# Performance work log

Hardware: AMD Instinct MI355X
Metric: run time of the kernel (lower is better)

The kernel has to match this reference:

```python
import jax, jax.numpy as jnp
import numpy as np

T, B, E = 1024, 4, 1024
H = 16
D = E // H          # head_dim = 64
L = 16              # max_relative_length


def setup_inputs() -> dict:
    key = jax.random.key(0)
    ks = jax.random.split(key, 4)
    query = jax.random.normal(ks[0], (T, B, E), dtype=jnp.float32)
    # xavier-ish scaled params
    in_proj_weight = jax.random.normal(ks[1], (3 * E, E), dtype=jnp.float32) * (1.0 / np.sqrt(E))
    in_proj_bias = jnp.zeros((3 * E,), dtype=jnp.float32)
    rel_pos_keys = jax.random.normal(ks[2], (2 * L + 1, E), dtype=jnp.float32) * (1.0 / np.sqrt(E))
    out_w = jax.random.normal(ks[3], (E, E), dtype=jnp.float32) * (1.0 / np.sqrt(E))
    out_b = jnp.zeros((E,), dtype=jnp.float32)
    return {"query": query, "in_proj_weight": in_proj_weight, "in_proj_bias": in_proj_bias,
            "rel_pos_keys": rel_pos_keys, "out_w": out_w, "out_b": out_b}


def reference(query, in_proj_weight, in_proj_bias, rel_pos_keys, out_w, out_b):
    t, b, e = query.shape
    scaling = D ** (-0.5)
    # fused qkv projection: [T,B,3E]
    qkv = jnp.einsum('tbe,fe->tbf', query, in_proj_weight) + in_proj_bias
    q, k, v = jnp.split(qkv, 3, axis=-1)
    q = q * scaling
    # [T,B,E] -> [B*H, T, D]
    def heads(x):
        return x.reshape(t, b * H, D).transpose(1, 0, 2)
    q, k, v = heads(q), heads(k), heads(v)
    # clipped relative position matrix [T,T] in [0, 2L]
    r = jnp.arange(t)
    dist = jnp.clip(r[None, :] - r[:, None], -L, L) + L
    # gather relation keys, keep first head_dim channels: [T,T,D]
    rel_k = rel_pos_keys[dist][:, :, :D]
    # scores = q k^T + q . rel_k  (Shaw et al.), [B*H, T, T]
    scores = jnp.einsum('btd,bsd->bts', q, k) + jnp.einsum('btd,tsd->bts', q, rel_k)
    probs = jax.nn.softmax(scores, axis=-1)
    attn = jnp.einsum('bts,bsd->btd', probs, v)      # [B*H, T, D]
    attn = attn.transpose(1, 0, 2).reshape(t, b, e)   # [T, B, E]
    return jnp.einsum('tbe,oe->tbo', attn, out_w) + out_b
```

## Files before the change

kernel.cpp:

```cpp
#include <hip/hip_runtime.h>

typedef __attribute__((ext_vector_type(8))) short short8;
typedef __attribute__((ext_vector_type(4))) float floatx4;


__device__ __forceinline__ short f2bf(float x) {
  union { float f; unsigned u; } cv; cv.f = x;
  unsigned u = cv.u + (0x7FFFu + ((cv.u >> 16) & 1u));
  return (short)(u >> 16);
}

__device__ __forceinline__ floatx4 mfma16(short8 a, short8 b, floatx4 c) {
  return __builtin_amdgcn_mfma_f32_16x16x32_bf16(a, b, c, 0, 0, 0);
}

__device__ __forceinline__ void async_copy16(const void* g, void* l) {
  __builtin_amdgcn_global_load_lds((const __attribute__((address_space(1))) void*)g,
                                   (__attribute__((address_space(3))) void*)l, 16, 0, 0);
}

__global__ void __launch_bounds__(256) convert_all_kernel(
    const float* __restrict__ s0, const float* __restrict__ s1,
    const float* __restrict__ s2,
    short* __restrict__ d0, short* __restrict__ d1, short* __restrict__ d2)
{
  int i = blockIdx.x * 256 + threadIdx.x;
  const float* src; short* dst; int off;
  if (i < 524288)       { src = s0; dst = d0; off = i; }
  else if (i < 917504)  { src = s1; dst = d1; off = i - 524288; }
  else                  { src = s2; dst = d2; off = i - 917504; }
  const float4* s = (const float4*)src;
  float4 a = s[off * 2], b = s[off * 2 + 1];
  short8 o;
  o[0] = f2bf(a.x); o[1] = f2bf(a.y); o[2] = f2bf(a.z); o[3] = f2bf(a.w);
  o[4] = f2bf(b.x); o[5] = f2bf(b.y); o[6] = f2bf(b.z); o[7] = f2bf(b.w);
  *(short8*)(dst + (size_t)off * 8) = o;
}

__device__ __forceinline__ void gemm_stage(
    const short* __restrict__ A, const short* __restrict__ W,
    short* Atile, short* Btile, int m0, int n0, int K, int kk, int tid, int w)
{
  #pragma unroll
  for (int i = 0; i < 2; i++) {
    int seg = i * 256 + tid;
    int row = seg >> 2, c = seg & 3;
    async_copy16(A + (size_t)(m0 + row) * K + kk + c * 8,
                 Atile + (size_t)(i * 256 + w * 64) * 8);
    async_copy16(W + (size_t)(n0 + row) * K + kk + c * 8,
                 Btile + (size_t)(i * 256 + w * 64) * 8);
  }
}

__device__ __forceinline__ void gemm_core_db(
    const short* __restrict__ A, const short* __restrict__ W,
    short* At, short* Bt,
    int m0, int n0, int K, int tid, floatx4 acc[4][4])
{
  const int lane = tid & 63, w = tid >> 6;
  const int quad = lane >> 4, l16 = lane & 15;
  const int wm = (w >> 1) * 64, wn = (w & 1) * 64;
  #pragma unroll
  for (int mt = 0; mt < 4; mt++)
    #pragma unroll
    for (int nt = 0; nt < 4; nt++) acc[mt][nt] = (floatx4)(0.0f);

  gemm_stage(A, W, At, Bt, m0, n0, K, 0, tid, w);

  for (int kk = 0; kk < K; kk += 32) {
    const int cur = (kk >> 5) & 1;
    short* Ac = At + cur * (128 * 32);
    short* Bc = Bt + cur * (128 * 32);
    __syncthreads();
    if (kk + 32 < K)
      gemm_stage(A, W, At + (1 - cur) * (128 * 32), Bt + (1 - cur) * (128 * 32),
                 m0, n0, K, kk + 32, tid, w);
    short8 af[4], bfr[4];
    #pragma unroll
    for (int mt = 0; mt < 4; mt++)
      af[mt] = *(const short8*)(Ac + (wm + mt * 16 + l16) * 32 + quad * 8);
    #pragma unroll
    for (int nt = 0; nt < 4; nt++)
      bfr[nt] = *(const short8*)(Bc + (wn + nt * 16 + l16) * 32 + quad * 8);
    #pragma unroll
    for (int mt = 0; mt < 4; mt++)
      #pragma unroll
      for (int nt = 0; nt < 4; nt++)
        acc[mt][nt] = mfma16(af[mt], bfr[nt], acc[mt][nt]);
  }
}

__global__ void __launch_bounds__(256) gemm_qkv(
    const short* __restrict__ A, const short* __restrict__ W,
    const float* __restrict__ bias,
    short* __restrict__ q_ws, short* __restrict__ k_ws, short* __restrict__ v_ws)
{
  __shared__ __align__(16) short Atile[2 * 128 * 32];
  __shared__ __align__(16) short Btile[2 * 128 * 32];
  const int tid = threadIdx.x;
  const int m0 = blockIdx.x * 128, n0 = blockIdx.y * 128;
  floatx4 acc[4][4];
  gemm_core_db(A, W, Atile, Btile, m0, n0, 1024, tid, acc);

  const int lane = tid & 63, w = tid >> 6;
  const int quad = lane >> 4, l16 = lane & 15;
  const int wm = (w >> 1) * 64, wn = (w & 1) * 64;
  #pragma unroll
  for (int nt = 0; nt < 4; nt++) {
    int f = n0 + wn + nt * 16 + l16;
    float bv = bias[f];
    int which = f >> 10;
    int h = (f >> 6) & 15;
    int d = f & 63;
    #pragma unroll
    for (int mt = 0; mt < 4; mt++) {
      #pragma unroll
      for (int reg = 0; reg < 4; reg++) {
        int r = m0 + wm + mt * 16 + quad * 4 + reg;
        int t = r >> 2, b = r & 3;
        int bh = b * 16 + h;
        float val = acc[mt][nt][reg] + bv;
        if (which == 0)      q_ws[((size_t)bh * 1024 + t) * 64 + d] = f2bf(val * 0.125f);
        else if (which == 1) k_ws[((size_t)bh * 1024 + t) * 64 + d] = f2bf(val);
        else                 v_ws[((size_t)bh * 64 + d) * 1024 + t] = f2bf(val);
      }
    }
  }
}

__global__ void __launch_bounds__(256) attn_kernel(
    const short* __restrict__ q_ws, const short* __restrict__ k_ws,
    const short* __restrict__ v_ws, const float* __restrict__ relk,
    short* __restrict__ attn_ws)
{
  __shared__ float rel_lds[64 * 33];
  __shared__ __align__(16) short Ktile[2][64 * 64];
  __shared__ __align__(16) short Vtile[2][64 * 64];
  __shared__ __align__(16) short p_lds[4][16 * 64];
  const int tid = threadIdx.x, lane = tid & 63, w = tid >> 6;
  const int quad = lane >> 4, l16 = lane & 15;
  const int bh = blockIdx.x >> 4;
  const int t0 = (blockIdx.x & 15) * 64;
  const int b = bh >> 4, h = bh & 15;

  short8 aq[2];
  #pragma unroll
  for (int ks = 0; ks < 2; ks++)
    aq[ks] = *(const short8*)(q_ws + ((size_t)bh * 1024 + t0 + w * 16 + l16) * 64
                              + ks * 32 + quad * 8);

  for (int i = tid; i < 48 * 8; i += 256) {
    int row = i >> 3, p = i & 7;
    short8 val;
    if (row < 33) {
      const float* src = relk + row * 1024 + p * 8;
      float4 a = *(const float4*)src, c = *(const float4*)(src + 4);
      val[0] = f2bf(a.x); val[1] = f2bf(a.y); val[2] = f2bf(a.z); val[3] = f2bf(a.w);
      val[4] = f2bf(c.x); val[5] = f2bf(c.y); val[6] = f2bf(c.z); val[7] = f2bf(c.w);
    } else {
      val = (short8)0;
    }
    *(short8*)(Ktile[0] + row * 64 + ((p ^ (row & 7)) << 3)) = val;
  }
  __syncthreads();

  #pragma unroll
  for (int jt = 0; jt < 3; jt++) {
    floatx4 scR = (floatx4)(0.0f);
    #pragma unroll
    for (int ks = 0; ks < 2; ks++) {
      int rrow = jt * 16 + l16;
      int ck = (quad + 4 * ks) ^ (rrow & 7);
      short8 rb = *(const short8*)(Ktile[0] + rrow * 64 + ck * 8);
      scR = mfma16(aq[ks], rb, scR);
    }
    int j = jt * 16 + l16;
    if (j < 33) {
      #pragma unroll
      for (int reg = 0; reg < 4; reg++) {
        int tl = w * 16 + quad * 4 + reg;
        rel_lds[tl * 33 + j] = scR[reg];
      }
    }
  }
  __syncthreads();

  const int qloc = w * 16 + l16;
  const float biasLo = rel_lds[qloc * 33 + 0];
  const float biasHi = rel_lds[qloc * 33 + 32];

  floatx4 o[4];
  #pragma unroll
  for (int dt = 0; dt < 4; dt++) o[dt] = (floatx4)(0.0f);
  float rsum = 0.f;

  const short* kg = k_ws + (size_t)bh * 1024 * 64;
  const short* vg = v_ws + (size_t)bh * 64 * 1024;

  #define STAGE_KV(S0, BUF)                                                  \
    {                                                                        \
      _Pragma("unroll")                                                      \
      for (int i = 0; i < 2; i++) {                                          \
        int seg = i * 256 + tid;                                             \
        int row = seg >> 3, p = seg & 7;                                     \
        int ck = p ^ (row & 7);                                              \
        async_copy16(kg + (size_t)((S0) + row) * 64 + ck * 8,                \
                     Ktile[BUF] + (size_t)(i * 256 + w * 64) * 8);           \
        async_copy16(vg + (size_t)row * 1024 + (S0) + ck * 8,                \
                     Vtile[BUF] + (size_t)(i * 256 + w * 64) * 8);           \
      }                                                                      \
    }

  STAGE_KV(0, 0);

  for (int st = 0; st < 16; st++) {
    const int s0 = st * 64;
    const int cur = st & 1;
    __syncthreads();
    if (st < 15) STAGE_KV(s0 + 64, 1 - cur);

    floatx4 sc[4];
    #pragma unroll
    for (int nt = 0; nt < 4; nt++) {
      sc[nt] = (floatx4)(0.0f);
      #pragma unroll
      for (int ks = 0; ks < 2; ks++) {
        int srow = nt * 16 + l16;
        int ck = (quad + 4 * ks) ^ (l16 & 7);
        short8 kb = *(const short8*)(Ktile[cur] + srow * 64 + ck * 8);
        sc[nt] = mfma16(kb, aq[ks], sc[nt]);
      }
    }

    bool alllo = (s0 <= t0 + w * 16 - 79);
    bool allhi = (s0 >= t0 + w * 16 + 31);
    if (alllo || allhi) {
      float bb = alllo ? biasLo : biasHi;
      #pragma unroll
      for (int nt = 0; nt < 4; nt++)
        #pragma unroll
        for (int reg = 0; reg < 4; reg++) sc[nt][reg] += bb;
    } else {
      #pragma unroll
      for (int nt = 0; nt < 4; nt++) {
        #pragma unroll
        for (int reg = 0; reg < 4; reg++) {
          int delta = (s0 + 16 * nt + 4 * quad + reg) - (t0 + qloc);
          delta = min(max(delta, -16), 16) + 16;
          sc[nt][reg] += rel_lds[qloc * 33 + delta];
        }
      }
    }

    #pragma unroll
    for (int nt = 0; nt < 4; nt++) {
      #pragma unroll
      for (int reg = 0; reg < 4; reg++) {
        float p = __expf(sc[nt][reg]);
        sc[nt][reg] = p;
        rsum += p;
      }
      unsigned w0 = (unsigned)(unsigned short)f2bf(sc[nt][0])
                  | ((unsigned)(unsigned short)f2bf(sc[nt][1]) << 16);
      unsigned w1 = (unsigned)(unsigned short)f2bf(sc[nt][2])
                  | ((unsigned)(unsigned short)f2bf(sc[nt][3]) << 16);
      int srot = (16 * nt + 4 * quad + 4 * l16) & 63;
      *(uint2*)(p_lds[w] + l16 * 64 + srot) = make_uint2(w0, w1);
    }

    short8 ap[2];
    #pragma unroll
    for (int ks = 0; ks < 2; ks++) {
      int s1 = (32 * ks + 8 * quad + 4 * l16) & 63;
      int s2 = (s1 + 4) & 63;
      union { short8 v; uint2 u[2]; } pu;
      pu.u[0] = *(const uint2*)(p_lds[w] + l16 * 64 + s1);
      pu.u[1] = *(const uint2*)(p_lds[w] + l16 * 64 + s2);
      ap[ks] = pu.v;
    }

    #pragma unroll
    for (int dt = 0; dt < 4; dt++) {
      #pragma unroll
      for (int ks = 0; ks < 2; ks++) {
        int drow = dt * 16 + l16;
        int ck = (quad + 4 * ks) ^ (l16 & 7);
        short8 vb = *(const short8*)(Vtile[cur] + drow * 64 + ck * 8);
        o[dt] = mfma16(ap[ks], vb, o[dt]);
      }
    }
  }
  #undef STAGE_KV

  rsum += __shfl_xor(rsum, 16, 64);
  rsum += __shfl_xor(rsum, 32, 64);
  float inv[4];
  #pragma unroll
  for (int reg = 0; reg < 4; reg++)
    inv[reg] = 1.0f / __shfl(rsum, quad * 4 + reg, 64);
  #pragma unroll
  for (int dt = 0; dt < 4; dt++) {
    #pragma unroll
    for (int reg = 0; reg < 4; reg++) {
      int tg = t0 + w * 16 + quad * 4 + reg;
      attn_ws[((size_t)tg * 4 + b) * 1024 + h * 64 + dt * 16 + l16]
        = f2bf(o[dt][reg] * inv[reg]);
    }
  }
}

__global__ void __launch_bounds__(256) gemm_outproj(
    const short* __restrict__ A, const short* __restrict__ W,
    const float* __restrict__ bias, float* __restrict__ out)
{
  __shared__ __align__(16) short Atile[2 * 64 * 32];
  __shared__ __align__(16) short Btile[2 * 128 * 32];
  const int tid = threadIdx.x;
  const int m0 = blockIdx.x * 64, n0 = blockIdx.y * 128;
  const int lane = tid & 63, w = tid >> 6;
  const int quad = lane >> 4, l16 = lane & 15;
  const int wm = (w >> 1) * 32, wn = (w & 1) * 64;

  floatx4 acc[2][4];
  #pragma unroll
  for (int mt = 0; mt < 2; mt++)
    #pragma unroll
    for (int nt = 0; nt < 4; nt++) acc[mt][nt] = (floatx4)(0.0f);

  #define STAGE_OP(KK, BUF)                                                  \
    {                                                                        \
      _Pragma("unroll")                                                      \
      for (int i = 0; i < 2; i++) {                                          \
        int seg = i * 256 + tid;                \
        int row = seg >> 2, c = seg & 3;                                     \
        async_copy16(W + (size_t)(n0 + row) * 1024 + (KK) + c * 8,           \
                     Btile + (size_t)((BUF) * 4096 + (i * 256 + w * 64) * 8)); \
      }                                                                      \
      {                                                                      \
        int row = tid >> 2, c = tid & 3;         \
        async_copy16(A + (size_t)(m0 + row) * 1024 + (KK) + c * 8,           \
                     Atile + (size_t)((BUF) * 2048 + (w * 64) * 8));         \
      }                                                                      \
    }

  STAGE_OP(0, 0);
  for (int kk = 0; kk < 1024; kk += 32) {
    const int cur = (kk >> 5) & 1;
    const short* Ac = Atile + cur * 2048;
    const short* Bc = Btile + cur * 4096;
    __syncthreads();
    if (kk + 32 < 1024) STAGE_OP(kk + 32, 1 - cur);
    short8 af[2], bfr[4];
    #pragma unroll
    for (int mt = 0; mt < 2; mt++)
      af[mt] = *(const short8*)(Ac + (wm + mt * 16 + l16) * 32 + quad * 8);
    #pragma unroll
    for (int nt = 0; nt < 4; nt++)
      bfr[nt] = *(const short8*)(Bc + (wn + nt * 16 + l16) * 32 + quad * 8);
    #pragma unroll
    for (int mt = 0; mt < 2; mt++)
      #pragma unroll
      for (int nt = 0; nt < 4; nt++)
        acc[mt][nt] = mfma16(af[mt], bfr[nt], acc[mt][nt]);
  }
  #undef STAGE_OP

  #pragma unroll
  for (int nt = 0; nt < 4; nt++) {
    int f = n0 + wn + nt * 16 + l16;
    float bv = bias[f];
    #pragma unroll
    for (int mt = 0; mt < 2; mt++) {
      #pragma unroll
      for (int reg = 0; reg < 4; reg++) {
        int r = m0 + wm + mt * 16 + quad * 4 + reg;
        out[(size_t)r * 1024 + f] = acc[mt][nt][reg] + bv;
      }
    }
  }
}

extern "C" void kernel_launch(void* const* d_in, const int* in_sizes, int n_in,
                              void* d_out, int out_size, void* d_ws, size_t ws_size,
                              hipStream_t stream) {
  const float* query = (const float*)d_in[0];
  const float* in_w  = (const float*)d_in[1];
  const float* in_b  = (const float*)d_in[2];
  const float* relk  = (const float*)d_in[3];
  const float* out_w = (const float*)d_in[4];
  const float* out_b = (const float*)d_in[5];
  float* out = (float*)d_out;

  short* qry_bf = (short*)d_ws;
  short* win_bf = qry_bf + (size_t)4096 * 1024;
  short* wout_bf = win_bf + (size_t)3072 * 1024;
  short* q_ws   = wout_bf + (size_t)1024 * 1024;
  short* k_ws   = q_ws + (size_t)64 * 1024 * 64;
  short* v_ws   = k_ws + (size_t)64 * 1024 * 64;
  short* att_ws = v_ws + (size_t)64 * 1024 * 64;

  convert_all_kernel<<<4096, 256, 0, stream>>>(query, in_w, out_w,
                                               qry_bf, win_bf, wout_bf);
  gemm_qkv<<<dim3(32, 24), 256, 0, stream>>>(qry_bf, win_bf, in_b, q_ws, k_ws, v_ws);
  attn_kernel<<<1024, 256, 0, stream>>>(q_ws, k_ws, v_ws, relk, att_ws);
  gemm_outproj<<<dim3(64, 8), 256, 0, stream>>>(att_ws, wout_bf, out_b, out);
}
```

Baseline: 188.6 us.

## Double query rows per attention block and swizzle GEMM LDS tiles

The attention kernel now handles 128 query rows per block (two 16-row tiles per wave), so each K/V tile loaded into LDS feeds twice as many MFMAs, and the grid drops to 512 blocks. K/V double buffering is removed in favour of a single buffer with a sync at the end of each iteration, which serialises the loads with compute. Separately, both GEMMs apply a rotation swizzle to LDS tile columns to reduce bank conflicts on fragment reads. The trade-offs are higher register pressure, fewer blocks, and lost load/compute overlap in attention.

```diff
diff --git a/kernel.cpp b/kernel.cpp
--- a/kernel.cpp
+++ b/kernel.cpp
@@ -44,10 +44,11 @@
   #pragma unroll
   for (int i = 0; i < 2; i++) {
     int seg = i * 256 + tid;
-    int row = seg >> 2, c = seg & 3;
-    async_copy16(A + (size_t)(m0 + row) * K + kk + c * 8,
+    int row = seg >> 2, p = seg & 3;
+    int ck = (p - ((row >> 1) & 3)) & 3;
+    async_copy16(A + (size_t)(m0 + row) * K + kk + ck * 8,
                  Atile + (size_t)(i * 256 + w * 64) * 8);
-    async_copy16(W + (size_t)(n0 + row) * K + kk + c * 8,
+    async_copy16(W + (size_t)(n0 + row) * K + kk + ck * 8,
                  Btile + (size_t)(i * 256 + w * 64) * 8);
   }
 }
@@ -77,11 +78,15 @@
                  m0, n0, K, kk + 32, tid, w);
     short8 af[4], bfr[4];
     #pragma unroll
-    for (int mt = 0; mt < 4; mt++)
-      af[mt] = *(const short8*)(Ac + (wm + mt * 16 + l16) * 32 + quad * 8);
-    #pragma unroll
-    for (int nt = 0; nt < 4; nt++)
-      bfr[nt] = *(const short8*)(Bc + (wn + nt * 16 + l16) * 32 + quad * 8);
+    for (int mt = 0; mt < 4; mt++) {
+      int R = wm + mt * 16 + l16;
+      af[mt] = *(const short8*)(Ac + R * 32 + ((quad + (R >> 1)) & 3) * 8);
+    }
+    #pragma unroll
+    for (int nt = 0; nt < 4; nt++) {
+      int R = wn + nt * 16 + l16;
+      bfr[nt] = *(const short8*)(Bc + R * 32 + ((quad + (R >> 1)) & 3) * 8);
+    }
     #pragma unroll
     for (int mt = 0; mt < 4; mt++)
       #pragma unroll
@@ -133,21 +138,24 @@
     const short* __restrict__ v_ws, const float* __restrict__ relk,
     short* __restrict__ attn_ws)
 {
-  __shared__ float rel_lds[64 * 33];
-  __shared__ __align__(16) short Ktile[2][64 * 64];
-  __shared__ __align__(16) short Vtile[2][64 * 64];
-  __shared__ __align__(16) short p_lds[4][16 * 64];
+  __shared__ float rel_lds[128 * 33];
+  __shared__ __align__(16) short Ktile[64 * 64];
+  __shared__ __align__(16) short Vtile[64 * 64];
+  __shared__ __align__(16) short p_lds[4][32 * 64];
   const int tid = threadIdx.x, lane = tid & 63, w = tid >> 6;
   const int quad = lane >> 4, l16 = lane & 15;
-  const int bh = blockIdx.x >> 4;
-  const int t0 = (blockIdx.x & 15) * 64;
+  const int bh = blockIdx.x >> 3;
+  const int t0 = (blockIdx.x & 7) * 128;
   const int b = bh >> 4, h = bh & 15;
 
-  short8 aq[2];
-  #pragma unroll
-  for (int ks = 0; ks < 2; ks++)
-    aq[ks] = *(const short8*)(q_ws + ((size_t)bh * 1024 + t0 + w * 16 + l16) * 64
-                              + ks * 32 + quad * 8);
+  short8 aq[2][2];
+  #pragma unroll
+  for (int qt = 0; qt < 2; qt++)
+    #pragma unroll
+    for (int ks = 0; ks < 2; ks++)
+      aq[qt][ks] = *(const short8*)(q_ws
+          + ((size_t)bh * 1024 + t0 + qt * 64 + w * 16 + l16) * 64
+          + ks * 32 + quad * 8);
 
   for (int i = tid; i < 48 * 8; i += 256) {
     int row = i >> 3, p = i & 7;
@@ -160,151 +168,174 @@
     } else {
       val = (short8)0;
     }
-    *(short8*)(Ktile[0] + row * 64 + ((p ^ (row & 7)) << 3)) = val;
+    *(short8*)(Ktile + row * 64 + ((p ^ (row & 7)) << 3)) = val;
   }
   __syncthreads();
 
   #pragma unroll
-  for (int jt = 0; jt < 3; jt++) {
-    floatx4 scR = (floatx4)(0.0f);
-    #pragma unroll
-    for (int ks = 0; ks < 2; ks++) {
-      int rrow = jt * 16 + l16;
-      int ck = (quad + 4 * ks) ^ (rrow & 7);
-      short8 rb = *(const short8*)(Ktile[0] + rrow * 64 + ck * 8);
-      scR = mfma16(aq[ks], rb, scR);
-    }
-    int j = jt * 16 + l16;
-    if (j < 33) {
-      #pragma unroll
-      for (int reg = 0; reg < 4; reg++) {
-        int tl = w * 16 + quad * 4 + reg;
-        rel_lds[tl * 33 + j] = scR[reg];
+  for (int qt = 0; qt < 2; qt++) {
+    #pragma unroll
+    for (int jt = 0; jt < 3; jt++) {
+      floatx4 scR = (floatx4)(0.0f);
+      #pragma unroll
+      for (int ks = 0; ks < 2; ks++) {
+        int rrow = jt * 16 + l16;
+        int ck = (quad + 4 * ks) ^ (rrow & 7);
+        short8 rb = *(const short8*)(Ktile + rrow * 64 + ck * 8);
+        scR = mfma16(aq[qt][ks], rb, scR);
+      }
+      int j = jt * 16 + l16;
+      if (j < 33) {
+        #pragma unroll
+        for (int reg = 0; reg < 4; reg++) {
+          int tl = qt * 64 + w * 16 + quad * 4 + reg;
+          rel_lds[tl * 33 + j] = scR[reg];
+        }
       }
     }
   }
   __syncthreads();
 
-  const int qloc = w * 16 + l16;
-  const float biasLo = rel_lds[qloc * 33 + 0];
-  const float biasHi = rel_lds[qloc * 33 + 32];
-
-  floatx4 o[4];
-  #pragma unroll
-  for (int dt = 0; dt < 4; dt++) o[dt] = (floatx4)(0.0f);
-  float rsum = 0.f;
+  float biasLo[2], biasHi[2];
+  #pragma unroll
+  for (int qt = 0; qt < 2; qt++) {
+    int ql = qt * 64 + w * 16 + l16;
+    biasLo[qt] = rel_lds[ql * 33 + 0];
+    biasHi[qt] = rel_lds[ql * 33 + 32];
+  }
+
+  floatx4 o[2][4];
+  #pragma unroll
+  for (int qt = 0; qt < 2; qt++)
+    #pragma unroll
+    for (int dt = 0; dt < 4; dt++) o[qt][dt] = (floatx4)(0.0f);
+  float rsum[2] = {0.f, 0.f};
 
   const short* kg = k_ws + (size_t)bh * 1024 * 64;
   const short* vg = v_ws + (size_t)bh * 64 * 1024;
 
-  #define STAGE_KV(S0, BUF)                                                  \
-    {                                                                        \
-      _Pragma("unroll")                                                      \
-      for (int i = 0; i < 2; i++) {                                          \
-        int seg = i * 256 + tid;                                             \
-        int row = seg >> 3, p = seg & 7;                                     \
-        int ck = p ^ (row & 7);                                              \
-        async_copy16(kg + (size_t)((S0) + row) * 64 + ck * 8,                \
-                     Ktile[BUF] + (size_t)(i * 256 + w * 64) * 8);           \
-        async_copy16(vg + (size_t)row * 1024 + (S0) + ck * 8,                \
-                     Vtile[BUF] + (size_t)(i * 256 + w * 64) * 8);           \
-      }                                                                      \
-    }
-
-  STAGE_KV(0, 0);
-
   for (int st = 0; st < 16; st++) {
     const int s0 = st * 64;
-    const int cur = st & 1;
+    #pragma unroll
+    for (int i = 0; i < 2; i++) {
+      int seg = i * 256 + tid;
+      int row = seg >> 3, p = seg & 7;
+      int ck = p ^ (row & 7);
+      async_copy16(kg + (size_t)(s0 + row) * 64 + ck * 8,
+                   Ktile + (size_t)(i * 256 + w * 64) * 8);
+      async_copy16(vg + (size_t)row * 1024 + s0 + ck * 8,
+                   Vtile + (size_t)(i * 256 + w * 64) * 8);
+    }
     __syncthreads();
-    if (st < 15) STAGE_KV(s0 + 64, 1 - cur);
-
-    floatx4 sc[4];
-    #pragma unroll
-    for (int nt = 0; nt < 4; nt++) {
-      sc[nt] = (floatx4)(0.0f);
+
+    short8 kb[4][2];
+    #pragma unroll
+    for (int nt = 0; nt < 4; nt++)
       #pragma unroll
       for (int ks = 0; ks < 2; ks++) {
         int srow = nt * 16 + l16;
-        int ck = (quad + 4 * ks) ^ (l16 & 7);
-        short8 kb = *(const short8*)(Ktile[cur] + srow * 64 + ck * 8);
-        sc[nt] = mfma16(kb, aq[ks], sc[nt]);
-      }
-    }
-
-    bool alllo = (s0 <= t0 + w * 16 - 79);
-    bool allhi = (s0 >= t0 + w * 16 + 31);
-    if (alllo || allhi) {
-      float bb = alllo ? biasLo : biasHi;
-      #pragma unroll
-      for (int nt = 0; nt < 4; nt++)
-        #pragma unroll
-        for (int reg = 0; reg < 4; reg++) sc[nt][reg] += bb;
-    } else {
+        kb[nt][ks] = *(const short8*)(Ktile + srow * 64
+                                      + (((quad + 4 * ks) ^ (l16 & 7)) << 3));
+      }
+
+    floatx4 sc[2][4];
+    #pragma unroll
+    for (int qt = 0; qt < 2; qt++)
       #pragma unroll
       for (int nt = 0; nt < 4; nt++) {
+        sc[qt][nt] = (floatx4)(0.0f);
+        #pragma unroll
+        for (int ks = 0; ks < 2; ks++)
+          sc[qt][nt] = mfma16(kb[nt][ks], aq[qt][ks], sc[qt][nt]);
+      }
+
+    #pragma unroll
+    for (int qt = 0; qt < 2; qt++) {
+      const int qbase = t0 + qt * 64 + w * 16;
+      bool alllo = (s0 <= qbase - 79);
+      bool allhi = (s0 >= qbase + 31);
+      if (alllo || allhi) {
+        float bb = alllo ? biasLo[qt] : biasHi[qt];
+        #pragma unroll
+        for (int nt = 0; nt < 4; nt++)
+          #pragma unroll
+          for (int reg = 0; reg < 4; reg++) sc[qt][nt][reg] += bb;
+      } else {
+        int ql = qt * 64 + w * 16 + l16;
+        #pragma unroll
+        for (int nt = 0; nt < 4; nt++)
+          #pragma unroll
+          for (int reg = 0; reg < 4; reg++) {
+            int delta = (s0 + 16 * nt + 4 * quad + reg) - (qbase + l16);
+            delta = min(max(delta, -16), 16) + 16;
+            sc[qt][nt][reg] += rel_lds[ql * 33 + delta];
+          }
+      }
+      #pragma unroll
+      for (int nt = 0; nt < 4; nt++) {
         #pragma unroll
         for (int reg = 0; reg < 4; reg++) {
-          int delta = (s0 + 16 * nt + 4 * quad + reg) - (t0 + qloc);
-          delta = min(max(delta, -16), 16) + 16;
-          sc[nt][reg] += rel_lds[qloc * 33 + delta];
+          float p = __expf(sc[qt][nt][reg]);
+          sc[qt][nt][reg] = p;
+          rsum[qt] += p;
         }
-      }
-    }
-
-    #pragma unroll
-    for (int nt = 0; nt < 4; nt++) {
-      #pragma unroll
-      for (int reg = 0; reg < 4; reg++) {
-        float p = __expf(sc[nt][reg]);
-        sc[nt][reg] = p;
-        rsum += p;
-      }
-      unsigned w0 = (unsigned)(unsigned short)f2bf(sc[nt][0])
-                  | ((unsigned)(unsigned short)f2bf(sc[nt][1]) << 16);
-      unsigned w1 = (unsigned)(unsigned short)f2bf(sc[nt][2])
-                  | ((unsigned)(unsigned short)f2bf(sc[nt][3]) << 16);
-      int srot = (16 * nt + 4 * quad + 4 * l16) & 63;
-      *(uint2*)(p_lds[w] + l16 * 64 + srot) = make_uint2(w0, w1);
-    }
-
-    short8 ap[2];
-    #pragma unroll
-    for (int ks = 0; ks < 2; ks++) {
-      int s1 = (32 * ks + 8 * quad + 4 * l16) & 63;
-      int s2 = (s1 + 4) & 63;
-      union { short8 v; uint2 u[2]; } pu;
-      pu.u[0] = *(const uint2*)(p_lds[w] + l16 * 64 + s1);
-      pu.u[1] = *(const uint2*)(p_lds[w] + l16 * 64 + s2);
-      ap[ks] = pu.v;
-    }
+        unsigned w0 = (unsigned)(unsigned short)f2bf(sc[qt][nt][0])
+                    | ((unsigned)(unsigned short)f2bf(sc[qt][nt][1]) << 16);
+        unsigned w1 = (unsigned)(unsigned short)f2bf(sc[qt][nt][2])
+                    | ((unsigned)(unsigned short)f2bf(sc[qt][nt][3]) << 16);
+        int srot = (16 * nt + 4 * quad + 4 * l16) & 63;
+        *(uint2*)(p_lds[w] + (qt * 16 + l16) * 64 + srot) = make_uint2(w0, w1);
+      }
+    }
+
+    short8 ap[2][2];
+    #pragma unroll
+    for (int qt = 0; qt < 2; qt++)
+      #pragma unroll
+      for (int ks = 0; ks < 2; ks++) {
+        int s1 = (32 * ks + 8 * quad + 4 * l16) & 63;
+        int s2 = (s1 + 4) & 63;
+        union { short8 v; uint2 u[2]; } pu;
+        pu.u[0] = *(const uint2*)(p_lds[w] + (qt * 16 + l16) * 64 + s1);
+        pu.u[1] = *(const uint2*)(p_lds[w] + (qt * 16 + l16) * 64 + s2);
+        ap[qt][ks] = pu.v;
+      }
 
     #pragma unroll
     for (int dt = 0; dt < 4; dt++) {
+      short8 vb[2];
       #pragma unroll
       for (int ks = 0; ks < 2; ks++) {
         int drow = dt * 16 + l16;
-        int ck = (quad + 4 * ks) ^ (l16 & 7);
-        short8 vb = *(const short8*)(Vtile[cur] + drow * 64 + ck * 8);
-        o[dt] = mfma16(ap[ks], vb, o[dt]);
-      }
-    }
-  }
-  #undef STAGE_KV
-
-  rsum += __shfl_xor(rsum, 16, 64);
-  rsum += __shfl_xor(rsum, 32, 64);
-  float inv[4];
-  #pragma unroll
-  for (int reg = 0; reg < 4; reg++)
-    inv[reg] = 1.0f / __shfl(rsum, quad * 4 + reg, 64);
-  #pragma unroll
-  for (int dt = 0; dt < 4; dt++) {
-    #pragma unroll
-    for (int reg = 0; reg < 4; reg++) {
-      int tg = t0 + w * 16 + quad * 4 + reg;
-      attn_ws[((size_t)tg * 4 + b) * 1024 + h * 64 + dt * 16 + l16]
-        = f2bf(o[dt][reg] * inv[reg]);
+        vb[ks] = *(const short8*)(Vtile + drow * 64
+                                  + (((quad + 4 * ks) ^ (l16 & 7)) << 3));
+      }
+      #pragma unroll
+      for (int qt = 0; qt < 2; qt++)
+        #pragma unroll
+        for (int ks = 0; ks < 2; ks++)
+          o[qt][dt] = mfma16(ap[qt][ks], vb[ks], o[qt][dt]);
+    }
+    __syncthreads();
+  }
+
+  #pragma unroll
+  for (int qt = 0; qt < 2; qt++) {
+    float rs = rsum[qt];
+    rs += __shfl_xor(rs, 16, 64);
+    rs += __shfl_xor(rs, 32, 64);
+    float inv[4];
+    #pragma unroll
+    for (int reg = 0; reg < 4; reg++)
+      inv[reg] = 1.0f / __shfl(rs, quad * 4 + reg, 64);
+    #pragma unroll
+    for (int dt = 0; dt < 4; dt++) {
+      #pragma unroll
+      for (int reg = 0; reg < 4; reg++) {
+        int tg = t0 + qt * 64 + w * 16 + quad * 4 + reg;
+        attn_ws[((size_t)tg * 4 + b) * 1024 + h * 64 + dt * 16 + l16]
+          = f2bf(o[qt][dt][reg] * inv[reg]);
+      }
     }
   }
 }
@@ -332,13 +363,15 @@
       _Pragma("unroll")                                                      \
       for (int i = 0; i < 2; i++) {                                          \
         int seg = i * 256 + tid;                \
-        int row = seg >> 2, c = seg & 3;                                     \
-        async_copy16(W + (size_t)(n0 + row) * 1024 + (KK) + c * 8,           \
+        int row = seg >> 2, p = seg & 3;                                     \
+        int ck = (p - ((row >> 1) & 3)) & 3;                                 \
+        async_copy16(W + (size_t)(n0 + row) * 1024 + (KK) + ck * 8,          \
                      Btile + (size_t)((BUF) * 4096 + (i * 256 + w * 64) * 8)); \
       }                                                                      \
       {                                                                      \
-        int row = tid >> 2, c = tid & 3;         \
-        async_copy16(A + (size_t)(m0 + row) * 1024 + (KK) + c * 8,           \
+        int row = tid >> 2, p = tid & 3;         \
+        int ck = (p - ((row >> 1) & 3)) & 3;                                 \
+        async_copy16(A + (size_t)(m0 + row) * 1024 + (KK) + ck * 8,          \
                      Atile + (size_t)((BUF) * 2048 + (w * 64) * 8));         \
       }                                                                      \
     }
@@ -352,11 +385,15 @@
     if (kk + 32 < 1024) STAGE_OP(kk + 32, 1 - cur);
     short8 af[2], bfr[4];
     #pragma unroll
-    for (int mt = 0; mt < 2; mt++)
-      af[mt] = *(const short8*)(Ac + (wm + mt * 16 + l16) * 32 + quad * 8);
-    #pragma unroll
-    for (int nt = 0; nt < 4; nt++)
-      bfr[nt] = *(const short8*)(Bc + (wn + nt * 16 + l16) * 32 + quad * 8);
+    for (int mt = 0; mt < 2; mt++) {
+      int R = wm + mt * 16 + l16;
+      af[mt] = *(const short8*)(Ac + R * 32 + ((quad + (R >> 1)) & 3) * 8);
+    }
+    #pragma unroll
+    for (int nt = 0; nt < 4; nt++) {
+      int R = wn + nt * 16 + l16;
+      bfr[nt] = *(const short8*)(Bc + R * 32 + ((quad + (R >> 1)) & 3) * 8);
+    }
     #pragma unroll
     for (int mt = 0; mt < 2; mt++)
       #pragma unroll
@@ -402,6 +439,6 @@
   convert_all_kernel<<<4096, 256, 0, stream>>>(query, in_w, out_w,
                                                qry_bf, win_bf, wout_bf);
   gemm_qkv<<<dim3(32, 24), 256, 0, stream>>>(qry_bf, win_bf, in_b, q_ws, k_ws, v_ws);
-  attn_kernel<<<1024, 256, 0, stream>>>(q_ws, k_ws, v_ws, relk, att_ws);
+  attn_kernel<<<512, 256, 0, stream>>>(q_ws, k_ws, v_ws, relk, att_ws);
   gemm_outproj<<<dim3(64, 8), 256, 0, stream>>>(att_ws, wout_bf, out_b, out);
 }
```

Result: no change. 187.4 us (-0.6%).
